# Kernel optimization log

Hardware: AMD Instinct MI355X
Metric: run time of the kernel (lower is better)

## Reference

```python
import jax, jax.numpy as jnp
import numpy as np

EPS = 1e-5
V, D, S, B, H, DH, FF, LE, LD = 32000, 512, 1024, 2, 8, 64, 2048, 2, 2


def _ln(x, g, b):
    m = x.mean(-1, keepdims=True)
    v = ((x - m) ** 2).mean(-1, keepdims=True)
    return (x - m) * jax.lax.rsqrt(v + EPS) * g + b


def _mha(qi, ki, vi, wq, wk, wv, uw, ub, mask):
    # wq/wk/wv: [H, D, DH] stacked per-head no-bias projections (concat order == head order)
    q = jnp.einsum('bsd,hde->bhse', qi, wq)
    k = jnp.einsum('btd,hde->bhte', ki, wk)
    v = jnp.einsum('btd,hde->bhte', vi, wv)
    scale = float(wq.shape[-1]) ** 0.5  # FAITHFUL to source: scores are MULTIPLIED by sqrt(d_head)
    s = jnp.einsum('bhse,bhte->bhst', q, k) * scale
    s = jnp.where(mask, s, -jnp.inf)  # causal tril mask applied in every attention (incl. cross)
    a = jax.nn.softmax(s, axis=-1)
    o = jnp.einsum('bhst,bhte->bhse', a, v)
    b_, h_, s_, e_ = o.shape
    o = o.transpose(0, 2, 1, 3).reshape(b_, s_, h_ * e_)
    return o @ uw + ub


def _posenc(seq, d):
    pos = jnp.arange(seq, dtype=jnp.float32)[:, None]
    den = jnp.exp(jnp.arange(0, d, 2, dtype=jnp.float32) * (-np.log(10000.0) / d))
    pe = jnp.zeros((seq, d), jnp.float32)
    pe = pe.at[:, 0::2].set(jnp.sin(pos * den))
    pe = pe.at[:, 1::2].set(jnp.cos(pos * den))
    return pe


def _forward(tokens, emb, enc_wq, enc_wk, enc_wv, enc_uo_w, enc_uo_b,
             enc_ln1_g, enc_ln1_b, enc_ln2_g, enc_ln2_b,
             enc_ff_w1, enc_ff_b1, enc_ff_w2, enc_ff_b2,
             dec_sa_wq, dec_sa_wk, dec_sa_wv, dec_sa_uo_w, dec_sa_uo_b,
             dec_ca_wq, dec_ca_wk, dec_ca_wv, dec_ca_uo_w, dec_ca_uo_b,
             dec_ln1_g, dec_ln1_b, dec_ln2_g, dec_ln2_b, dec_ln3_g, dec_ln3_b,
             dec_ff_w1, dec_ff_b1, dec_ff_w2, dec_ff_b2,
             ln_enc_g, ln_enc_b, ln_dec_g, ln_dec_b, head_w, head_b):
    b, s = tokens.shape
    d = emb.shape[1]
    x = emb[tokens] + _posenc(s, d)  # [B, S, D]
    mask = jnp.tril(jnp.ones((s, s), bool))
    enc = jax.lax.stop_gradient(x)  # source: x.detach().clone()
    for l in range(enc_wq.shape[0]):
        h = _ln(enc, enc_ln1_g[l], enc_ln1_b[l])
        enc = enc + _mha(h, h, h, enc_wq[l], enc_wk[l], enc_wv[l], enc_uo_w[l], enc_uo_b[l], mask)
        h = _ln(enc, enc_ln2_g[l], enc_ln2_b[l])
        enc = enc + (jnp.maximum(h @ enc_ff_w1[l] + enc_ff_b1[l], 0.0) @ enc_ff_w2[l] + enc_ff_b2[l])
    enc = _ln(enc, ln_enc_g, ln_enc_b)
    for l in range(dec_sa_wq.shape[0]):
        h = _ln(x, dec_ln1_g[l], dec_ln1_b[l])
        x = x + _mha(h, h, h, dec_sa_wq[l], dec_sa_wk[l], dec_sa_wv[l], dec_sa_uo_w[l], dec_sa_uo_b[l], mask)
        h = _ln(x, dec_ln2_g[l], dec_ln2_b[l])
        x = x + _mha(h, enc, enc, dec_ca_wq[l], dec_ca_wk[l], dec_ca_wv[l], dec_ca_uo_w[l], dec_ca_uo_b[l], mask)
        h = _ln(x, dec_ln3_g[l], dec_ln3_b[l])
        x = x + (jnp.maximum(h @ dec_ff_w1[l] + dec_ff_b1[l], 0.0) @ dec_ff_w2[l] + dec_ff_b2[l])
    x = _ln(x, ln_dec_g, ln_dec_b)
    return x @ head_w + head_b  # [B, S, V]


def setup_inputs():
    key = jax.random.key(0)
    ks = iter(jax.random.split(key, 64))
    def n(shape):
        return jax.random.normal(next(ks), shape, jnp.float32) * 0.02
    return {
        'tokens': jax.random.randint(next(ks), (B, S), 0, V, jnp.int32),
        'emb': n((V, D)),
        'enc_wq': n((LE, H, D, DH)), 'enc_wk': n((LE, H, D, DH)), 'enc_wv': n((LE, H, D, DH)),
        'enc_uo_w': n((LE, D, D)), 'enc_uo_b': jnp.zeros((LE, D), jnp.float32),
        'enc_ln1_g': jnp.ones((LE, D), jnp.float32), 'enc_ln1_b': jnp.zeros((LE, D), jnp.float32),
        'enc_ln2_g': jnp.ones((LE, D), jnp.float32), 'enc_ln2_b': jnp.zeros((LE, D), jnp.float32),
        'enc_ff_w1': n((LE, D, FF)), 'enc_ff_b1': jnp.zeros((LE, FF), jnp.float32),
        'enc_ff_w2': n((LE, FF, D)), 'enc_ff_b2': jnp.zeros((LE, D), jnp.float32),
        'dec_sa_wq': n((LD, H, D, DH)), 'dec_sa_wk': n((LD, H, D, DH)), 'dec_sa_wv': n((LD, H, D, DH)),
        'dec_sa_uo_w': n((LD, D, D)), 'dec_sa_uo_b': jnp.zeros((LD, D), jnp.float32),
        'dec_ca_wq': n((LD, H, D, DH)), 'dec_ca_wk': n((LD, H, D, DH)), 'dec_ca_wv': n((LD, H, D, DH)),
        'dec_ca_uo_w': n((LD, D, D)), 'dec_ca_uo_b': jnp.zeros((LD, D), jnp.float32),
        'dec_ln1_g': jnp.ones((LD, D), jnp.float32), 'dec_ln1_b': jnp.zeros((LD, D), jnp.float32),
        'dec_ln2_g': jnp.ones((LD, D), jnp.float32), 'dec_ln2_b': jnp.zeros((LD, D), jnp.float32),
        'dec_ln3_g': jnp.ones((LD, D), jnp.float32), 'dec_ln3_b': jnp.zeros((LD, D), jnp.float32),
        'dec_ff_w1': n((LD, D, FF)), 'dec_ff_b1': jnp.zeros((LD, FF), jnp.float32),
        'dec_ff_w2': n((LD, FF, D)), 'dec_ff_b2': jnp.zeros((LD, D), jnp.float32),
        'ln_enc_g': jnp.ones((D,), jnp.float32), 'ln_enc_b': jnp.zeros((D,), jnp.float32),
        'ln_dec_g': jnp.ones((D,), jnp.float32), 'ln_dec_b': jnp.zeros((D,), jnp.float32),
        'head_w': n((D, V)), 'head_b': jnp.zeros((V,), jnp.float32),
    }


def reference(tokens, emb, enc_wq, enc_wk, enc_wv, enc_uo_w, enc_uo_b,
              enc_ln1_g, enc_ln1_b, enc_ln2_g, enc_ln2_b,
              enc_ff_w1, enc_ff_b1, enc_ff_w2, enc_ff_b2,
              dec_sa_wq, dec_sa_wk, dec_sa_wv, dec_sa_uo_w, dec_sa_uo_b,
              dec_ca_wq, dec_ca_wk, dec_ca_wv, dec_ca_uo_w, dec_ca_uo_b,
              dec_ln1_g, dec_ln1_b, dec_ln2_g, dec_ln2_b, dec_ln3_g, dec_ln3_b,
              dec_ff_w1, dec_ff_b1, dec_ff_w2, dec_ff_b2,
              ln_enc_g, ln_enc_b, ln_dec_g, ln_dec_b, head_w, head_b):
    return _forward(tokens, emb, enc_wq, enc_wk, enc_wv, enc_uo_w, enc_uo_b,
                    enc_ln1_g, enc_ln1_b, enc_ln2_g, enc_ln2_b,
                    enc_ff_w1, enc_ff_b1, enc_ff_w2, enc_ff_b2,
                    dec_sa_wq, dec_sa_wk, dec_sa_wv, dec_sa_uo_w, dec_sa_uo_b,
                    dec_ca_wq, dec_ca_wk, dec_ca_wv, dec_ca_uo_w, dec_ca_uo_b,
                    dec_ln1_g, dec_ln1_b, dec_ln2_g, dec_ln2_b, dec_ln3_g, dec_ln3_b,
                    dec_ff_w1, dec_ff_b1, dec_ff_w2, dec_ff_b2,
                    ln_enc_g, ln_enc_b, ln_dec_g, ln_dec_b, head_w, head_b)
```

## Files before the change

kernel.cpp:

```cpp
#include <hip/hip_runtime.h>
#include <cstddef>
#include <cstdint>

constexpr int Vv = 32000, Dd = 512, Ss = 1024, Bb = 2, Hh = 8, DHd = 64, FFf = 2048;
constexpr int Tt = Bb * Ss;
constexpr int QKVW = 3 * Dd;
constexpr float EPSf = 1e-5f;

typedef unsigned short ushort_t;
typedef short bf16x8 __attribute__((ext_vector_type(8)));
typedef short short4v __attribute__((ext_vector_type(4)));
typedef float f32x4 __attribute__((ext_vector_type(4)));

constexpr size_t AQKV = 0;
constexpr size_t AUO  = 4718592;
constexpr size_t AFF1 = 6291456;
constexpr size_t AFF2 = 10485760;
constexpr size_t AEND = 14680064;

__device__ __forceinline__ ushort_t f2b(float f) {
  unsigned int u = __float_as_uint(f);
  unsigned int r = (u + 0x7FFFu + ((u >> 16) & 1u)) >> 16;
  return (ushort_t)r;
}
__device__ __forceinline__ float bits2f(ushort_t u) {
  return __uint_as_float((unsigned int)u << 16);
}

__device__ __forceinline__ void st_out(float* p, float v) { *p = v; }
__device__ __forceinline__ void st_out(ushort_t* p, float v) { *p = f2b(v); }

__device__ __forceinline__ void gload_lds16(const void* g, void* l) {
  __builtin_amdgcn_global_load_lds(
      (const __attribute__((address_space(1))) unsigned int*)g,
      (__attribute__((address_space(3))) unsigned int*)l, 16, 0, 0);
}

__global__ __launch_bounds__(256) void prep_all_k(
    const float* __restrict__ ewq, const float* __restrict__ ewk, const float* __restrict__ ewv,
    const float* __restrict__ swq, const float* __restrict__ swk, const float* __restrict__ swv,
    const float* __restrict__ cwq, const float* __restrict__ cwk, const float* __restrict__ cwv,
    const float* __restrict__ euo, const float* __restrict__ suo, const float* __restrict__ cuo,
    const float* __restrict__ eff1, const float* __restrict__ dff1,
    const float* __restrict__ eff2, const float* __restrict__ dff2,
    ushort_t* __restrict__ arena,
    const int* __restrict__ tok, const float* __restrict__ emb,
    float* __restrict__ X, float* __restrict__ ENC,
    const float* __restrict__ headw, ushort_t* __restrict__ headDst) {
  int idx = blockIdx.x;

  if (idx >= 14336 && idx < 16384) {
    int row = idx - 14336;
    int s = row & (Ss - 1);
    int t = tok[row];
    const float* e = emb + (size_t)t * Dd;
    for (int d = threadIdx.x; d < Dd; d += 256) {
      int i = d >> 1;
      float den = expf(-(float)(2 * i) * (9.210340371976184f / 512.0f));
      float ang = (float)s * den;
      float pe = (d & 1) ? cosf(ang) : sinf(ang);
      float v = e[d] + pe;
      X[(size_t)row * Dd + d] = v;
      ENC[(size_t)row * Dd + d] = v;
    }
    return;
  }

  const float* src;
  ushort_t* dst;
  int R, C, tile;
  if (idx < 4608) {
    tile = idx & 31;
    int rest = idx >> 5;
    int h = rest & 7; rest >>= 3;
    int t = rest % 3, gl = rest / 3;
    int g = gl >> 1, l = gl & 1;
    const float* bq = (g == 0) ? ewq : (g == 1) ? swq : cwq;
    const float* bk = (g == 0) ? ewk : (g == 1) ? swk : cwk;
    const float* bv = (g == 0) ? ewv : (g == 1) ? swv : cwv;
    const float* base = (t == 0) ? bq : (t == 1) ? bk : bv;
    src = base + (size_t)l * (Hh * Dd * DHd) + (size_t)h * (Dd * DHd);
    dst = arena + AQKV + (size_t)gl * (QKVW * Dd) + ((size_t)t * Dd + h * DHd) * Dd;
    R = 512; C = 64;
  } else if (idx < 6144) {
    int i2 = idx - 4608;
    tile = i2 & 255;
    int gl = i2 >> 8;
    int g = gl >> 1, l = gl & 1;
    const float* base = (g == 0) ? euo : (g == 1) ? suo : cuo;
    src = base + (size_t)l * (Dd * Dd);
    dst = arena + AUO + (size_t)gl * (Dd * Dd);
    R = 512; C = 512;
  } else if (idx < 10240) {
    int i3 = idx - 6144;
    tile = i3 & 1023;
    int dl = i3 >> 10;
    int d = dl >> 1, l = dl & 1;
    src = (d ? dff1 : eff1) + (size_t)l * (Dd * FFf);
    dst = arena + AFF1 + (size_t)dl * (Dd * FFf);
    R = 512; C = 2048;
  } else if (idx < 14336) {
    int i4 = idx - 10240;
    tile = i4 & 1023;
    int dl = i4 >> 10;
    int d = dl >> 1, l = dl & 1;
    src = (d ? dff2 : eff2) + (size_t)l * (FFf * Dd);
    dst = arena + AFF2 + (size_t)dl * (FFf * Dd);
    R = 2048; C = 512;
  } else {
    tile = idx - 16384;
    src = headw; dst = headDst;
    R = 512; C = 32000;
  }
  int nR = R >> 5;
  int r0 = (tile % nR) * 32, c0 = (tile / nR) * 32;
  __shared__ float tb[32][33];
  int tx = threadIdx.x & 31, ty = threadIdx.x >> 5;
#pragma unroll
  for (int i = 0; i < 4; i++)
    tb[ty + i * 8][tx] = src[(size_t)(r0 + ty + i * 8) * C + c0 + tx];
  __syncthreads();
#pragma unroll
  for (int i = 0; i < 4; i++)
    dst[(size_t)(c0 + ty + i * 8) * R + r0 + tx] = f2b(tb[tx][ty + i * 8]);
}

__global__ __launch_bounds__(256) void tcast_k(const float* __restrict__ in,
                                               ushort_t* __restrict__ out,
                                               int R, int C) {
  __shared__ float t[32][33];
  int c0 = blockIdx.x * 32, r0 = blockIdx.y * 32;
  int tx = threadIdx.x & 31, ty = threadIdx.x >> 5;
#pragma unroll
  for (int i = 0; i < 4; i++)
    t[ty + i * 8][tx] = in[(size_t)(r0 + ty + i * 8) * C + c0 + tx];
  __syncthreads();
#pragma unroll
  for (int i = 0; i < 4; i++)
    out[(size_t)(c0 + ty + i * 8) * R + r0 + tx] = f2b(t[tx][ty + i * 8]);
}

__global__ __launch_bounds__(256) void ln2_k(const float* __restrict__ in0,
                                             const float* __restrict__ g0,
                                             const float* __restrict__ b0,
                                             ushort_t* __restrict__ o0,
                                             const float* __restrict__ in1,
                                             const float* __restrict__ g1,
                                             const float* __restrict__ b1,
                                             ushort_t* __restrict__ o1,
                                             int nblk0) {
  int row = blockIdx.x;
  const float* in = in0; const float* g = g0; const float* b = b0; ushort_t* out = o0;
  if (row >= nblk0) { row -= nblk0; in = in1; g = g1; b = b1; out = o1; }
  const float* x = in + (size_t)row * Dd;
  int tid = threadIdx.x;
  float v0 = x[tid], v1 = x[tid + 256];
  float s = v0 + v1, ss = v0 * v0 + v1 * v1;
  for (int o = 32; o; o >>= 1) {
    s  += __shfl_down(s, o, 64);
    ss += __shfl_down(ss, o, 64);
  }
  __shared__ float rs[4], rss[4];
  int wid = tid >> 6, lane = tid & 63;
  if (lane == 0) { rs[wid] = s; rss[wid] = ss; }
  __syncthreads();
  __shared__ float mean_s, inv_s;
  if (tid == 0) {
    float a = rs[0] + rs[1] + rs[2] + rs[3];
    float c = rss[0] + rss[1] + rss[2] + rss[3];
    float m = a / Dd;
    float var = c / Dd - m * m;
    mean_s = m;
    inv_s = rsqrtf(var + EPSf);
  }
  __syncthreads();
  float m = mean_s, inv = inv_s;
  out[(size_t)row * Dd + tid]       = f2b((v0 - m) * inv * g[tid]       + b[tid]);
  out[(size_t)row * Dd + tid + 256] = f2b((v1 - m) * inv * g[tid + 256] + b[tid + 256]);
}

__device__ __forceinline__ void block_coords(int o, int nwg, bool nmajor,
                                             int nbM, int nbN, int& bmOut, int& bnOut) {
  int q = nwg >> 3, r = nwg & 7;
  int x = o & 7, i = o >> 3;
  int l = (x < r ? x * (q + 1) : r * (q + 1) + (x - r) * q) + i;
  int mb, nb;
  if (nmajor) { mb = l % nbM; nb = l / nbM; }
  else        { nb = l % nbN; mb = l / nbN; }
  bmOut = mb; bnOut = nb;
}

struct GD {
  const ushort_t* A; const ushort_t* BT; const float* bias; const float* resid;
  void* C; int N; int K; int ldc; int nbM; int nbN; int nwg;
};

template <int BM, int BN, bool NMAJOR, typename OutT, bool RELU>
__global__ __launch_bounds__(256) void gemm2_k(GD d0, GD d1, int nblk0) {
  constexpr int FM = BM / 32, FN = BN / 32;
  __shared__ __align__(16) ushort_t As[BM * 64];
  __shared__ __align__(16) ushort_t Bs[BN * 64];

  GD d = d0;
  int o = blockIdx.x;
  if (o >= nblk0) { d = d1; o -= nblk0; }
  int mb, nb;
  block_coords(o, d.nwg, NMAJOR, d.nbM, d.nbN, mb, nb);
  int bm = mb * BM, bn = nb * BN;
  int K = d.K, ldc = d.ldc;
  OutT* C = (OutT*)d.C;

  int tid = threadIdx.x;
  int lane = tid & 63, w = tid >> 6;
  int wr = w >> 1, wc = w & 1;
  f32x4 acc[FM][FN];
#pragma unroll
  for (int m = 0; m < FM; m++)
#pragma unroll
    for (int n = 0; n < FN; n++) acc[m][n] = (f32x4){0.f, 0.f, 0.f, 0.f};

  const ushort_t* aBase = d.A + (size_t)bm * K;
  const ushort_t* bBase = d.BT + (size_t)bn * K;
  int lr = lane & 15;
  int lk = (lane >> 4) * 8;

  for (int k0 = 0; k0 < K; k0 += 64) {
    __syncthreads();
#pragma unroll
    for (int it = 0; it < BM / 32; it++) {
      int cid = it * 256 + tid;
      int row = cid >> 3, c8 = cid & 7;
      int sc8 = c8 ^ (row & 7);
      gload_lds16(aBase + (size_t)row * K + k0 + sc8 * 8, &As[cid * 8]);
    }
#pragma unroll
    for (int it = 0; it < BN / 32; it++) {
      int cid = it * 256 + tid;
      int row = cid >> 3, c8 = cid & 7;
      int sc8 = c8 ^ (row & 7);
      gload_lds16(bBase + (size_t)row * K + k0 + sc8 * 8, &Bs[cid * 8]);
    }
    __syncthreads();
#pragma unroll
    for (int kk = 0; kk < 64; kk += 32) {
      bf16x8 af[FM], bfr[FN];
#pragma unroll
      for (int m = 0; m < FM; m++) {
        int row = wr * (BM / 2) + m * 16 + lr;
        af[m] = *(const bf16x8*)&As[row * 64 + ((kk + lk) ^ ((row & 7) << 3))];
      }
#pragma unroll
      for (int n = 0; n < FN; n++) {
        int row = wc * (BN / 2) + n * 16 + lr;
        bfr[n] = *(const bf16x8*)&Bs[row * 64 + ((kk + lk) ^ ((row & 7) << 3))];
      }
#pragma unroll
      for (int m = 0; m < FM; m++)
#pragma unroll
        for (int n = 0; n < FN; n++)
          acc[m][n] = __builtin_amdgcn_mfma_f32_16x16x32_bf16(af[m], bfr[n], acc[m][n], 0, 0, 0);
    }
  }

  int rowg = (lane >> 4) * 4;
#pragma unroll
  for (int m = 0; m < FM; m++) {
    int row0 = bm + wr * (BM / 2) + m * 16 + rowg;
#pragma unroll
    for (int n = 0; n < FN; n++) {
      int col = bn + wc * (BN / 2) + n * 16 + lr;
      float bv = d.bias ? d.bias[col] : 0.0f;
#pragma unroll
      for (int rr = 0; rr < 4; rr++) {
        int row = row0 + rr;
        float v = acc[m][n][rr] + bv;
        if (d.resid) v += d.resid[(size_t)row * ldc + col];
        if (RELU)  v = fmaxf(v, 0.0f);
        st_out(&C[(size_t)row * ldc + col], v);
      }
    }
  }
}

__global__ __launch_bounds__(128) void fattn_k(const float* __restrict__ QKV0,
                                               ushort_t* __restrict__ AO0,
                                               const float* __restrict__ QKV1,
                                               ushort_t* __restrict__ AO1,
                                               int nblk0) {
  int bid = blockIdx.x;
  const float* QKV = QKV0; ushort_t* AO = AO0;
  if (bid >= nblk0) { bid -= nblk0; QKV = QKV1; AO = AO1; }
  int i4 = bid >> 4;
  int qt = (i4 < 16) ? (31 - i4) : (i4 - 16);
  int h  = bid & 7;
  int b  = (bid >> 3) & 1;
  int q0 = qt * 32;
  int tid = threadIdx.x;
  int lane = tid & 63, w = tid >> 6;
  int g = lane >> 4, c = lane & 15;

  __shared__ __align__(16) ushort_t Qh[32 * 64], Ql[32 * 64];
  __shared__ __align__(16) ushort_t Kh[64 * 64], Kl[64 * 64];
  __shared__ __align__(16) ushort_t VT[64 * 64];
  __shared__ __align__(16) ushort_t Ps[2][16 * 64];

  {
    int row = tid >> 2, c0 = (tid & 3) * 16;
    const float* qb = QKV + ((size_t)(b * Ss + q0 + row) * QKVW + h * DHd + c0);
#pragma unroll
    for (int ii = 0; ii < 4; ii++) {
      float4 v = *(const float4*)(qb + ii * 4);
      int col = c0 + ii * 4;
      int sc = col ^ ((row & 7) << 3);
      ushort_t h0 = f2b(v.x), h1 = f2b(v.y), h2 = f2b(v.z), h3 = f2b(v.w);
      short4v hv = {(short)h0, (short)h1, (short)h2, (short)h3};
      short4v lv = {(short)f2b(v.x - bits2f(h0)), (short)f2b(v.y - bits2f(h1)),
                    (short)f2b(v.z - bits2f(h2)), (short)f2b(v.w - bits2f(h3))};
      *(short4v*)&Qh[row * 64 + sc] = hv;
      *(short4v*)&Ql[row * 64 + sc] = lv;
    }
  }

  f32x4 Oa[4];
#pragma unroll
  for (int n = 0; n < 4; n++) Oa[n] = (f32x4){0.f, 0.f, 0.f, 0.f};
  float mrow[4] = {-INFINITY, -INFINITY, -INFINITY, -INFINITY};
  float lrow[4] = {0.f, 0.f, 0.f, 0.f};

  int nkv = (qt >> 1) + 1;
  for (int it = 0; it < nkv; it++) {
    int t0 = it * 64;
    __syncthreads();
    {
      int row = tid >> 1, c0 = (tid & 1) * 32;
      const float* kb = QKV + ((size_t)(b * Ss + t0 + row) * QKVW + Dd + h * DHd + c0);
      const float* vb = kb + Dd;
#pragma unroll
      for (int ii = 0; ii < 8; ii++) {
        float4 v = *(const float4*)(kb + ii * 4);
        int col = c0 + ii * 4;
        int sc = col ^ ((row & 7) << 3);
        ushort_t h0 = f2b(v.x), h1 = f2b(v.y), h2 = f2b(v.z), h3 = f2b(v.w);
        short4v hv = {(short)h0, (short)h1, (short)h2, (short)h3};
        short4v lv = {(short)f2b(v.x - bits2f(h0)), (short)f2b(v.y - bits2f(h1)),
                      (short)f2b(v.z - bits2f(h2)), (short)f2b(v.w - bits2f(h3))};
        *(short4v*)&Kh[row * 64 + sc] = hv;
        *(short4v*)&Kl[row * 64 + sc] = lv;
      }
#pragma unroll
      for (int ii = 0; ii < 8; ii++) {
        float4 v = *(const float4*)(vb + ii * 4);
        int e0 = c0 + ii * 4;
        VT[(e0 + 0) * 64 + (row ^ (((e0 + 0) & 7) << 3))] = f2b(v.x);
        VT[(e0 + 1) * 64 + (row ^ (((e0 + 1) & 7) << 3))] = f2b(v.y);
        VT[(e0 + 2) * 64 + (row ^ (((e0 + 2) & 7) << 3))] = f2b(v.z);
        VT[(e0 + 3) * 64 + (row ^ (((e0 + 3) & 7) << 3))] = f2b(v.w);
      }
    }
    __syncthreads();

    int arow = w * 16 + c;
    int ksw0 = (0 + g * 8) ^ ((c & 7) << 3);
    int ksw1 = (32 + g * 8) ^ ((c & 7) << 3);
    bf16x8 qh0 = *(const bf16x8*)&Qh[arow * 64 + ksw0];
    bf16x8 qh1 = *(const bf16x8*)&Qh[arow * 64 + ksw1];
    bf16x8 ql0 = *(const bf16x8*)&Ql[arow * 64 + ksw0];
    bf16x8 ql1 = *(const bf16x8*)&Ql[arow * 64 + ksw1];

    f32x4 sfr[4];
#pragma unroll
    for (int n = 0; n < 4; n++) {
      int brow = n * 16 + c;
      bf16x8 kh0 = *(const bf16x8*)&Kh[brow * 64 + ksw0];
      bf16x8 kh1 = *(const bf16x8*)&Kh[brow * 64 + ksw1];
      bf16x8 kl0 = *(const bf16x8*)&Kl[brow * 64 + ksw0];
      bf16x8 kl1 = *(const bf16x8*)&Kl[brow * 64 + ksw1];
      f32x4 a = (f32x4){0.f, 0.f, 0.f, 0.f};
      a = __builtin_amdgcn_mfma_f32_16x16x32_bf16(qh0, kl0, a, 0, 0, 0);
      a = __builtin_amdgcn_mfma_f32_16x16x32_bf16(qh1, kl1, a, 0, 0, 0);
      a = __builtin_amdgcn_mfma_f32_16x16x32_bf16(ql0, kh0, a, 0, 0, 0);
      a = __builtin_amdgcn_mfma_f32_16x16x32_bf16(ql1, kh1, a, 0, 0, 0);
      a = __builtin_amdgcn_mfma_f32_16x16x32_bf16(qh0, kh0, a, 0, 0, 0);
      a = __builtin_amdgcn_mfma_f32_16x16x32_bf16(qh1, kh1, a, 0, 0, 0);
      sfr[n] = a;
    }

#pragma unroll
    for (int n = 0; n < 4; n++) {
#pragma unroll
      for (int rr = 0; rr < 4; rr++) sfr[n][rr] *= 8.0f;
    }
    if (it == nkv - 1) {
#pragma unroll
      for (int n = 0; n < 4; n++) {
        int t = t0 + n * 16 + c;
#pragma unroll
        for (int rr = 0; rr < 4; rr++) {
          int s = q0 + w * 16 + g * 4 + rr;
          if (t > s) sfr[n][rr] = -INFINITY;
        }
      }
    }

    float pnew[4], scold[4];
#pragma unroll
    for (int rr = 0; rr < 4; rr++) {
      float tm = fmaxf(fmaxf(sfr[0][rr], sfr[1][rr]), fmaxf(sfr[2][rr], sfr[3][rr]));
      tm = fmaxf(tm, __shfl_xor(tm, 1));
      tm = fmaxf(tm, __shfl_xor(tm, 2));
      tm = fmaxf(tm, __shfl_xor(tm, 4));
      tm = fmaxf(tm, __shfl_xor(tm, 8));
      float mn = fmaxf(mrow[rr], tm);
      scold[rr] = __expf(mrow[rr] - mn);
      mrow[rr] = mn;
      pnew[rr] = mn;
    }
#pragma unroll
    for (int n = 0; n < 4; n++) {
#pragma unroll
      for (int rr = 0; rr < 4; rr++) sfr[n][rr] = __expf(sfr[n][rr] - pnew[rr]);
    }
#pragma unroll
    for (int rr = 0; rr < 4; rr++) {
      float s = sfr[0][rr] + sfr[1][rr] + sfr[2][rr] + sfr[3][rr];
      s += __shfl_xor(s, 1);
      s += __shfl_xor(s, 2);
      s += __shfl_xor(s, 4);
      s += __shfl_xor(s, 8);
      lrow[rr] = lrow[rr] * scold[rr] + s;
    }

#pragma unroll
    for (int n = 0; n < 4; n++) {
#pragma unroll
      for (int rr = 0; rr < 4; rr++) {
        int prow = g * 4 + rr;
        Ps[w][prow * 64 + ((n * 16 + c) ^ ((prow & 7) << 3))] = f2b(sfr[n][rr]);
      }
    }

#pragma unroll
    for (int n = 0; n < 4; n++) {
#pragma unroll
      for (int rr = 0; rr < 4; rr++) Oa[n][rr] *= scold[rr];
    }

    bf16x8 pa0 = *(const bf16x8*)&Ps[w][c * 64 + ksw0];
    bf16x8 pa1 = *(const bf16x8*)&Ps[w][c * 64 + ksw1];
#pragma unroll
    for (int n = 0; n < 4; n++) {
      int vrow = n * 16 + c;
      bf16x8 v0 = *(const bf16x8*)&VT[vrow * 64 + ksw0];
      bf16x8 v1 = *(const bf16x8*)&VT[vrow * 64 + ksw1];
      Oa[n] = __builtin_amdgcn_mfma_f32_16x16x32_bf16(pa0, v0, Oa[n], 0, 0, 0);
      Oa[n] = __builtin_amdgcn_mfma_f32_16x16x32_bf16(pa1, v1, Oa[n], 0, 0, 0);
    }
  }

#pragma unroll
  for (int rr = 0; rr < 4; rr++) {
    float inv = 1.0f / lrow[rr];
    int row = b * Ss + q0 + w * 16 + g * 4 + rr;
#pragma unroll
    for (int n = 0; n < 4; n++) {
      AO[(size_t)row * Dd + h * DHd + n * 16 + c] = f2b(Oa[n][rr] * inv);
    }
  }
}

static GD mkGD(const ushort_t* A, const ushort_t* BT, const float* bias,
               const float* resid, void* C, int M, int N, int K, int ldc,
               int BM, int BN) {
  GD d;
  d.A = A; d.BT = BT; d.bias = bias; d.resid = resid; d.C = C;
  d.N = N; d.K = K; d.ldc = ldc;
  d.nbM = M / BM; d.nbN = N / BN; d.nwg = d.nbM * d.nbN;
  return d;
}

template <int BM, int BN, bool NMAJOR, typename OutT, bool RELU>
static void gemm1(hipStream_t st, GD d) {
  gemm2_k<BM, BN, NMAJOR, OutT, RELU><<<dim3(d.nwg), dim3(256), 0, st>>>(d, d, d.nwg);
}
template <int BM, int BN, bool NMAJOR, typename OutT, bool RELU>
static void gemm2(hipStream_t st, GD d0, GD d1) {
  gemm2_k<BM, BN, NMAJOR, OutT, RELU><<<dim3(d0.nwg + d1.nwg), dim3(256), 0, st>>>(d0, d1, d0.nwg);
}

extern "C" void kernel_launch(void* const* d_in, const int* in_sizes, int n_in,
                              void* d_out, int out_size, void* d_ws, size_t ws_size,
                              hipStream_t stream) {
  const int*   tokens    = (const int*)d_in[0];
  const float* emb       = (const float*)d_in[1];
  const float* enc_wq    = (const float*)d_in[2];
  const float* enc_wk    = (const float*)d_in[3];
  const float* enc_wv    = (const float*)d_in[4];
  const float* enc_uo_w  = (const float*)d_in[5];
  const float* enc_uo_b  = (const float*)d_in[6];
  const float* enc_ln1_g = (const float*)d_in[7];
  const float* enc_ln1_b = (const float*)d_in[8];
  const float* enc_ln2_g = (const float*)d_in[9];
  const float* enc_ln2_b = (const float*)d_in[10];
  const float* enc_ff_w1 = (const float*)d_in[11];
  const float* enc_ff_b1 = (const float*)d_in[12];
  const float* enc_ff_w2 = (const float*)d_in[13];
  const float* enc_ff_b2 = (const float*)d_in[14];
  const float* dec_sa_wq = (const float*)d_in[15];
  const float* dec_sa_wk = (const float*)d_in[16];
  const float* dec_sa_wv = (const float*)d_in[17];
  const float* dec_sa_uo_w = (const float*)d_in[18];
  const float* dec_sa_uo_b = (const float*)d_in[19];
  const float* dec_ca_wq = (const float*)d_in[20];
  const float* dec_ca_wk = (const float*)d_in[21];
  const float* dec_ca_wv = (const float*)d_in[22];
  const float* dec_ca_uo_w = (const float*)d_in[23];
  const float* dec_ca_uo_b = (const float*)d_in[24];
  const float* dec_ln1_g = (const float*)d_in[25];
  const float* dec_ln1_b = (const float*)d_in[26];
  const float* dec_ln2_g = (const float*)d_in[27];
  const float* dec_ln2_b = (const float*)d_in[28];
  const float* dec_ln3_g = (const float*)d_in[29];
  const float* dec_ln3_b = (const float*)d_in[30];
  const float* dec_ff_w1 = (const float*)d_in[31];
  const float* dec_ff_b1 = (const float*)d_in[32];
  const float* dec_ff_w2 = (const float*)d_in[33];
  const float* dec_ff_b2 = (const float*)d_in[34];
  const float* ln_enc_g  = (const float*)d_in[35];
  const float* ln_enc_b  = (const float*)d_in[36];
  const float* ln_dec_g  = (const float*)d_in[37];
  const float* ln_dec_b  = (const float*)d_in[38];
  const float* head_w    = (const float*)d_in[39];
  const float* head_b    = (const float*)d_in[40];
  float* out = (float*)d_out;

  char* ws = (char*)d_ws;
  size_t off = 0;
  auto alloc = [&](size_t bytes) {
    void* p = ws + off;
    off += (bytes + 255) & ~(size_t)255;
    return p;
  };
  ushort_t* Hb    = (ushort_t*)alloc((size_t)Tt * Dd * 2);
  ushort_t* Hb2   = (ushort_t*)alloc((size_t)Tt * Dd * 2);
  ushort_t* ENCFb = (ushort_t*)alloc((size_t)Tt * Dd * 2);
  float*    X     = (float*)alloc((size_t)Tt * Dd * 4);
  float*    ENC   = (float*)alloc((size_t)Tt * Dd * 4);
  float*    QKV   = (float*)alloc((size_t)Tt * QKVW * 4);
  float*    QKV2  = (float*)alloc((size_t)Tt * QKVW * 4);
  ushort_t* AO    = (ushort_t*)alloc((size_t)Tt * Dd * 2);
  ushort_t* AO2   = (ushort_t*)alloc((size_t)Tt * Dd * 2);
  ushort_t* Fb    = (ushort_t*)alloc((size_t)Tt * FFf * 2);
  ushort_t* ARENA = (ushort_t*)alloc(AEND * 2);

  size_t headBytes = (size_t)Vv * Dd * 2;
  bool headInPrep = (off + headBytes) <= ws_size;
  ushort_t* BThead = headInPrep ? (ushort_t*)alloc(headBytes) : (ushort_t*)X;

  dim3 blk(256), fblk(128);
  int attnB = Bb * Hh * (Ss / 32);

  {
    int nprep = 14336 + 2048 + (headInPrep ? 16000 : 0);
    prep_all_k<<<nprep, blk, 0, stream>>>(
        enc_wq, enc_wk, enc_wv, dec_sa_wq, dec_sa_wk, dec_sa_wv,
        dec_ca_wq, dec_ca_wk, dec_ca_wv,
        enc_uo_w, dec_sa_uo_w, dec_ca_uo_w,
        enc_ff_w1, dec_ff_w1, enc_ff_w2, dec_ff_w2, ARENA,
        tokens, emb, X, ENC, head_w, headInPrep ? BThead : nullptr);
  }

  auto BTq  = [&](int gl) { return ARENA + AQKV + (size_t)gl * (QKVW * Dd); };
  auto BTu  = [&](int gl) { return ARENA + AUO  + (size_t)gl * (Dd * Dd); };
  auto BT1  = [&](int dl) { return ARENA + AFF1 + (size_t)dl * (Dd * FFf); };
  auto BT2  = [&](int dl) { return ARENA + AFF2 + (size_t)dl * (FFf * Dd); };

  ln2_k<<<2 * Tt, blk, 0, stream>>>(ENC, enc_ln1_g, enc_ln1_b, Hb,
                                    X, dec_ln1_g, dec_ln1_b, Hb2, Tt);
  gemm2<64, 128, true, float, false>(stream,
      mkGD(Hb,  BTq(0), nullptr, nullptr, QKV,  Tt, QKVW, Dd, QKVW, 64, 128),
      mkGD(Hb2, BTq(2), nullptr, nullptr, QKV2, Tt, QKVW, Dd, QKVW, 64, 128));
  fattn_k<<<2 * attnB, fblk, 0, stream>>>(QKV, AO, QKV2, AO2, attnB);
  gemm2<64, 64, true, float, false>(stream,
      mkGD(AO,  BTu(0), enc_uo_b,    ENC, ENC, Tt, Dd, Dd, Dd, 64, 64),
      mkGD(AO2, BTu(2), dec_sa_uo_b, X,   X,   Tt, Dd, Dd, Dd, 64, 64));
  ln2_k<<<Tt, blk, 0, stream>>>(ENC, enc_ln2_g, enc_ln2_b, Hb, ENC, enc_ln2_g, enc_ln2_b, Hb, Tt);
  gemm1<64, 128, true, ushort_t, true>(stream,
      mkGD(Hb, BT1(0), enc_ff_b1, nullptr, Fb, Tt, FFf, Dd, FFf, 64, 128));
  gemm1<64, 64, false, float, false>(stream,
      mkGD(Fb, BT2(0), enc_ff_b2, ENC, ENC, Tt, Dd, FFf, Dd, 64, 64));

  ln2_k<<<Tt, blk, 0, stream>>>(ENC, enc_ln1_g + Dd, enc_ln1_b + Dd, Hb,
                                ENC, enc_ln1_g + Dd, enc_ln1_b + Dd, Hb, Tt);
  gemm1<64, 128, true, float, false>(stream,
      mkGD(Hb, BTq(1), nullptr, nullptr, QKV, Tt, QKVW, Dd, QKVW, 64, 128));
  fattn_k<<<attnB, fblk, 0, stream>>>(QKV, AO, QKV, AO, attnB);
  gemm1<64, 64, true, float, false>(stream,
      mkGD(AO, BTu(1), enc_uo_b + Dd, ENC, ENC, Tt, Dd, Dd, Dd, 64, 64));
  ln2_k<<<Tt, blk, 0, stream>>>(ENC, enc_ln2_g + Dd, enc_ln2_b + Dd, Hb,
                                ENC, enc_ln2_g + Dd, enc_ln2_b + Dd, Hb, Tt);
  gemm1<64, 128, true, ushort_t, true>(stream,
      mkGD(Hb, BT1(1), enc_ff_b1 + FFf, nullptr, Fb, Tt, FFf, Dd, FFf, 64, 128));
  gemm1<64, 64, false, float, false>(stream,
      mkGD(Fb, BT2(1), enc_ff_b2 + Dd, ENC, ENC, Tt, Dd, FFf, Dd, 64, 64));

  for (int l = 0; l < 2; l++) {
    if (l == 0) {
      ln2_k<<<2 * Tt, blk, 0, stream>>>(ENC, ln_enc_g, ln_enc_b, ENCFb,
                                        X, dec_ln2_g, dec_ln2_b, Hb, Tt);
    } else {
      ln2_k<<<Tt, blk, 0, stream>>>(X, dec_ln1_g + Dd, dec_ln1_b + Dd, Hb,
                                    X, dec_ln1_g + Dd, dec_ln1_b + Dd, Hb, Tt);
      gemm1<64, 128, true, float, false>(stream,
          mkGD(Hb, BTq(3), nullptr, nullptr, QKV, Tt, QKVW, Dd, QKVW, 64, 128));
      fattn_k<<<attnB, fblk, 0, stream>>>(QKV, AO, QKV, AO, attnB);
      gemm1<64, 64, true, float, false>(stream,
          mkGD(AO, BTu(3), dec_sa_uo_b + Dd, X, X, Tt, Dd, Dd, Dd, 64, 64));
      ln2_k<<<Tt, blk, 0, stream>>>(X, dec_ln2_g + Dd, dec_ln2_b + Dd, Hb,
                                    X, dec_ln2_g + Dd, dec_ln2_b + Dd, Hb, Tt);
    }
    const ushort_t* BTca = BTq(4 + l);
    gemm2<64, 128, true, float, false>(stream,
        mkGD(Hb,    BTca,                    nullptr, nullptr, QKV,      Tt, Dd,     Dd, QKVW, 64, 128),
        mkGD(ENCFb, BTca + (size_t)Dd * Dd,  nullptr, nullptr, QKV + Dd, Tt, 2 * Dd, Dd, QKVW, 64, 128));
    fattn_k<<<attnB, fblk, 0, stream>>>(QKV, AO, QKV, AO, attnB);
    gemm1<64, 64, true, float, false>(stream,
        mkGD(AO, BTu(4 + l), dec_ca_uo_b + l * Dd, X, X, Tt, Dd, Dd, Dd, 64, 64));
    ln2_k<<<Tt, blk, 0, stream>>>(X, dec_ln3_g + l * Dd, dec_ln3_b + l * Dd, Hb,
                                  X, dec_ln3_g + l * Dd, dec_ln3_b + l * Dd, Hb, Tt);
    gemm1<64, 128, true, ushort_t, true>(stream,
        mkGD(Hb, BT1(2 + l), dec_ff_b1 + l * FFf, nullptr, Fb, Tt, FFf, Dd, FFf, 64, 128));
    gemm1<64, 64, false, float, false>(stream,
        mkGD(Fb, BT2(2 + l), dec_ff_b2 + l * Dd, X, X, Tt, Dd, FFf, Dd, 64, 64));
  }
  ln2_k<<<Tt, blk, 0, stream>>>(X, ln_dec_g, ln_dec_b, Hb, X, ln_dec_g, ln_dec_b, Hb, Tt);

  if (!headInPrep)
    tcast_k<<<dim3(Vv / 32, Dd / 32), blk, 0, stream>>>(head_w, BThead, Dd, Vv);
  gemm1<128, 128, true, float, false>(stream,
      mkGD(Hb, BThead, head_b, nullptr, out, Tt, Vv, Dd, Vv, 128, 128));
}
```

Measured before the change: 741.3 us.

## Widen GEMM K-tile and co-schedule encoder FFN with decoder cross-attn Q

The GEMM kernel gains a BK template parameter, and most projection and FFN GEMMs now use a 128-wide K tile, which halves the number of K-loop iterations and barriers. ReLU and bf16 output become runtime flags instead of template parameters, so different epilogues can share one launch. The decoder's first-layer cross-attention Q projection is now batched with the encoder's first FFN1 GEMM, and its LayerNorm is batched with the encoder ln2, which cuts launches and fills the GPU better. In exchange, shared memory per block doubles, which may lower occupancy, and the epilogue gains runtime branches.

Result: no change. 741.3 us (median of 2 runs) (-0.0%).

```diff
diff --git a/kernel.cpp b/kernel.cpp
--- a/kernel.cpp
+++ b/kernel.cpp
@@ -26,9 +26,6 @@
 __device__ __forceinline__ float bits2f(ushort_t u) {
   return __uint_as_float((unsigned int)u << 16);
 }
-
-__device__ __forceinline__ void st_out(float* p, float v) { *p = v; }
-__device__ __forceinline__ void st_out(ushort_t* p, float v) { *p = f2b(v); }
 
 __device__ __forceinline__ void gload_lds16(const void* g, void* l) {
   __builtin_amdgcn_global_load_lds(
@@ -192,14 +189,15 @@
 
 struct GD {
   const ushort_t* A; const ushort_t* BT; const float* bias; const float* resid;
-  void* C; int N; int K; int ldc; int nbM; int nbN; int nwg;
+  void* C; int N; int K; int ldc; int nbM; int nbN; int nwg; int relu; int obf16;
 };
 
-template <int BM, int BN, bool NMAJOR, typename OutT, bool RELU>
+template <int BM, int BN, int BK, bool NMAJOR>
 __global__ __launch_bounds__(256) void gemm2_k(GD d0, GD d1, int nblk0) {
   constexpr int FM = BM / 32, FN = BN / 32;
-  __shared__ __align__(16) ushort_t As[BM * 64];
-  __shared__ __align__(16) ushort_t Bs[BN * 64];
+  constexpr int KG = BK / 8;
+  __shared__ __align__(16) ushort_t As[BM * BK];
+  __shared__ __align__(16) ushort_t Bs[BN * BK];
 
   GD d = d0;
   int o = blockIdx.x;
@@ -208,7 +206,6 @@
   block_coords(o, d.nwg, NMAJOR, d.nbM, d.nbN, mb, nb);
   int bm = mb * BM, bn = nb * BN;
   int K = d.K, ldc = d.ldc;
-  OutT* C = (OutT*)d.C;
 
   int tid = threadIdx.x;
   int lane = tid & 63, w = tid >> 6;
@@ -224,35 +221,35 @@
   int lr = lane & 15;
   int lk = (lane >> 4) * 8;
 
-  for (int k0 = 0; k0 < K; k0 += 64) {
+  for (int k0 = 0; k0 < K; k0 += BK) {
     __syncthreads();
 #pragma unroll
-    for (int it = 0; it < BM / 32; it++) {
+    for (int it = 0; it < (BM * BK) / 2048; it++) {
       int cid = it * 256 + tid;
-      int row = cid >> 3, c8 = cid & 7;
+      int row = cid / KG, c8 = cid % KG;
       int sc8 = c8 ^ (row & 7);
       gload_lds16(aBase + (size_t)row * K + k0 + sc8 * 8, &As[cid * 8]);
     }
 #pragma unroll
-    for (int it = 0; it < BN / 32; it++) {
+    for (int it = 0; it < (BN * BK) / 2048; it++) {
       int cid = it * 256 + tid;
-      int row = cid >> 3, c8 = cid & 7;
+      int row = cid / KG, c8 = cid % KG;
       int sc8 = c8 ^ (row & 7);
       gload_lds16(bBase + (size_t)row * K + k0 + sc8 * 8, &Bs[cid * 8]);
     }
     __syncthreads();
 #pragma unroll
-    for (int kk = 0; kk < 64; kk += 32) {
+    for (int kk = 0; kk < BK; kk += 32) {
       bf16x8 af[FM], bfr[FN];
 #pragma unroll
       for (int m = 0; m < FM; m++) {
         int row = wr * (BM / 2) + m * 16 + lr;
-        af[m] = *(const bf16x8*)&As[row * 64 + ((kk + lk) ^ ((row & 7) << 3))];
+        af[m] = *(const bf16x8*)&As[row * BK + ((kk + lk) ^ ((row & 7) << 3))];
       }
 #pragma unroll
       for (int n = 0; n < FN; n++) {
         int row = wc * (BN / 2) + n * 16 + lr;
-        bfr[n] = *(const bf16x8*)&Bs[row * 64 + ((kk + lk) ^ ((row & 7) << 3))];
+        bfr[n] = *(const bf16x8*)&Bs[row * BK + ((kk + lk) ^ ((row & 7) << 3))];
       }
 #pragma unroll
       for (int m = 0; m < FM; m++)
@@ -275,8 +272,9 @@
         int row = row0 + rr;
         float v = acc[m][n][rr] + bv;
         if (d.resid) v += d.resid[(size_t)row * ldc + col];
-        if (RELU)  v = fmaxf(v, 0.0f);
-        st_out(&C[(size_t)row * ldc + col], v);
+        if (d.relu)  v = fmaxf(v, 0.0f);
+        if (d.obf16) ((ushort_t*)d.C)[(size_t)row * ldc + col] = f2b(v);
+        else         ((float*)d.C)[(size_t)row * ldc + col] = v;
       }
     }
   }
@@ -470,21 +468,22 @@
 
 static GD mkGD(const ushort_t* A, const ushort_t* BT, const float* bias,
                const float* resid, void* C, int M, int N, int K, int ldc,
-               int BM, int BN) {
+               int BM, int BN, int relu, int obf16) {
   GD d;
   d.A = A; d.BT = BT; d.bias = bias; d.resid = resid; d.C = C;
   d.N = N; d.K = K; d.ldc = ldc;
   d.nbM = M / BM; d.nbN = N / BN; d.nwg = d.nbM * d.nbN;
+  d.relu = relu; d.obf16 = obf16;
   return d;
 }
 
-template <int BM, int BN, bool NMAJOR, typename OutT, bool RELU>
+template <int BM, int BN, int BK, bool NMAJOR>
 static void gemm1(hipStream_t st, GD d) {
-  gemm2_k<BM, BN, NMAJOR, OutT, RELU><<<dim3(d.nwg), dim3(256), 0, st>>>(d, d, d.nwg);
-}
-template <int BM, int BN, bool NMAJOR, typename OutT, bool RELU>
+  gemm2_k<BM, BN, BK, NMAJOR><<<dim3(d.nwg), dim3(256), 0, st>>>(d, d, d.nwg);
+}
+template <int BM, int BN, int BK, bool NMAJOR>
 static void gemm2(hipStream_t st, GD d0, GD d1) {
-  gemm2_k<BM, BN, NMAJOR, OutT, RELU><<<dim3(d0.nwg + d1.nwg), dim3(256), 0, st>>>(d0, d1, d0.nwg);
+  gemm2_k<BM, BN, BK, NMAJOR><<<dim3(d0.nwg + d1.nwg), dim3(256), 0, st>>>(d0, d1, d0.nwg);
 }
 
 extern "C" void kernel_launch(void* const* d_in, const int* in_sizes, int n_in,
@@ -576,66 +575,76 @@
 
   ln2_k<<<2 * Tt, blk, 0, stream>>>(ENC, enc_ln1_g, enc_ln1_b, Hb,
                                     X, dec_ln1_g, dec_ln1_b, Hb2, Tt);
-  gemm2<64, 128, true, float, false>(stream,
-      mkGD(Hb,  BTq(0), nullptr, nullptr, QKV,  Tt, QKVW, Dd, QKVW, 64, 128),
-      mkGD(Hb2, BTq(2), nullptr, nullptr, QKV2, Tt, QKVW, Dd, QKVW, 64, 128));
+  gemm2<64, 128, 128, true>(stream,
+      mkGD(Hb,  BTq(0), nullptr, nullptr, QKV,  Tt, QKVW, Dd, QKVW, 64, 128, 0, 0),
+      mkGD(Hb2, BTq(2), nullptr, nullptr, QKV2, Tt, QKVW, Dd, QKVW, 64, 128, 0, 0));
   fattn_k<<<2 * attnB, fblk, 0, stream>>>(QKV, AO, QKV2, AO2, attnB);
-  gemm2<64, 64, true, float, false>(stream,
-      mkGD(AO,  BTu(0), enc_uo_b,    ENC, ENC, Tt, Dd, Dd, Dd, 64, 64),
-      mkGD(AO2, BTu(2), dec_sa_uo_b, X,   X,   Tt, Dd, Dd, Dd, 64, 64));
-  ln2_k<<<Tt, blk, 0, stream>>>(ENC, enc_ln2_g, enc_ln2_b, Hb, ENC, enc_ln2_g, enc_ln2_b, Hb, Tt);
-  gemm1<64, 128, true, ushort_t, true>(stream,
-      mkGD(Hb, BT1(0), enc_ff_b1, nullptr, Fb, Tt, FFf, Dd, FFf, 64, 128));
-  gemm1<64, 64, false, float, false>(stream,
-      mkGD(Fb, BT2(0), enc_ff_b2, ENC, ENC, Tt, Dd, FFf, Dd, 64, 64));
+  gemm2<64, 64, 128, true>(stream,
+      mkGD(AO,  BTu(0), enc_uo_b,    ENC, ENC, Tt, Dd, Dd, Dd, 64, 64, 0, 0),
+      mkGD(AO2, BTu(2), dec_sa_uo_b, X,   X,   Tt, Dd, Dd, Dd, 64, 64, 0, 0));
+  ln2_k<<<2 * Tt, blk, 0, stream>>>(ENC, enc_ln2_g, enc_ln2_b, Hb,
+                                    X, dec_ln2_g, dec_ln2_b, Hb2, Tt);
+  gemm2<64, 128, 128, true>(stream,
+      mkGD(Hb,  BT1(0), enc_ff_b1, nullptr, Fb,   Tt, FFf, Dd, FFf,  64, 128, 1, 1),
+      mkGD(Hb2, BTq(4), nullptr,   nullptr, QKV2, Tt, Dd,  Dd, QKVW, 64, 128, 0, 0));
+  gemm1<64, 64, 128, false>(stream,
+      mkGD(Fb, BT2(0), enc_ff_b2, ENC, ENC, Tt, Dd, FFf, Dd, 64, 64, 0, 0));
 
   ln2_k<<<Tt, blk, 0, stream>>>(ENC, enc_ln1_g + Dd, enc_ln1_b + Dd, Hb,
                                 ENC, enc_ln1_g + Dd, enc_ln1_b + Dd, Hb, Tt);
-  gemm1<64, 128, true, float, false>(stream,
-      mkGD(Hb, BTq(1), nullptr, nullptr, QKV, Tt, QKVW, Dd, QKVW, 64, 128));
+  gemm1<64, 128, 128, true>(stream,
+      mkGD(Hb, BTq(1), nullptr, nullptr, QKV, Tt, QKVW, Dd, QKVW, 64, 128, 0, 0));
   fattn_k<<<attnB, fblk, 0, stream>>>(QKV, AO, QKV, AO, attnB);
-  gemm1<64, 64, true, float, false>(stream,
-      mkGD(AO, BTu(1), enc_uo_b + Dd, ENC, ENC, Tt, Dd, Dd, Dd, 64, 64));
+  gemm1<64, 64, 128, true>(stream,
+      mkGD(AO, BTu(1), enc_uo_b + Dd, ENC, ENC, Tt, Dd, Dd, Dd, 64, 64, 0, 0));
   ln2_k<<<Tt, blk, 0, stream>>>(ENC, enc_ln2_g + Dd, enc_ln2_b + Dd, Hb,
                                 ENC, enc_ln2_g + Dd, enc_ln2_b + Dd, Hb, Tt);
-  gemm1<64, 128, true, ushort_t, true>(stream,
-      mkGD(Hb, BT1(1), enc_ff_b1 + FFf, nullptr, Fb, Tt, FFf, Dd, FFf, 64, 128));
-  gemm1<64, 64, false, float, false>(stream,
-      mkGD(Fb, BT2(1), enc_ff_b2 + Dd, ENC, ENC, Tt, Dd, FFf, Dd, 64, 64));
-
-  for (int l = 0; l < 2; l++) {
-    if (l == 0) {
-      ln2_k<<<2 * Tt, blk, 0, stream>>>(ENC, ln_enc_g, ln_enc_b, ENCFb,
-                                        X, dec_ln2_g, dec_ln2_b, Hb, Tt);
-    } else {
-      ln2_k<<<Tt, blk, 0, stream>>>(X, dec_ln1_g + Dd, dec_ln1_b + Dd, Hb,
-                                    X, dec_ln1_g + Dd, dec_ln1_b + Dd, Hb, Tt);
-      gemm1<64, 128, true, float, false>(stream,
-          mkGD(Hb, BTq(3), nullptr, nullptr, QKV, Tt, QKVW, Dd, QKVW, 64, 128));
-      fattn_k<<<attnB, fblk, 0, stream>>>(QKV, AO, QKV, AO, attnB);
-      gemm1<64, 64, true, float, false>(stream,
-          mkGD(AO, BTu(3), dec_sa_uo_b + Dd, X, X, Tt, Dd, Dd, Dd, 64, 64));
-      ln2_k<<<Tt, blk, 0, stream>>>(X, dec_ln2_g + Dd, dec_ln2_b + Dd, Hb,
-                                    X, dec_ln2_g + Dd, dec_ln2_b + Dd, Hb, Tt);
-    }
-    const ushort_t* BTca = BTq(4 + l);
-    gemm2<64, 128, true, float, false>(stream,
-        mkGD(Hb,    BTca,                    nullptr, nullptr, QKV,      Tt, Dd,     Dd, QKVW, 64, 128),
-        mkGD(ENCFb, BTca + (size_t)Dd * Dd,  nullptr, nullptr, QKV + Dd, Tt, 2 * Dd, Dd, QKVW, 64, 128));
-    fattn_k<<<attnB, fblk, 0, stream>>>(QKV, AO, QKV, AO, attnB);
-    gemm1<64, 64, true, float, false>(stream,
-        mkGD(AO, BTu(4 + l), dec_ca_uo_b + l * Dd, X, X, Tt, Dd, Dd, Dd, 64, 64));
-    ln2_k<<<Tt, blk, 0, stream>>>(X, dec_ln3_g + l * Dd, dec_ln3_b + l * Dd, Hb,
-                                  X, dec_ln3_g + l * Dd, dec_ln3_b + l * Dd, Hb, Tt);
-    gemm1<64, 128, true, ushort_t, true>(stream,
-        mkGD(Hb, BT1(2 + l), dec_ff_b1 + l * FFf, nullptr, Fb, Tt, FFf, Dd, FFf, 64, 128));
-    gemm1<64, 64, false, float, false>(stream,
-        mkGD(Fb, BT2(2 + l), dec_ff_b2 + l * Dd, X, X, Tt, Dd, FFf, Dd, 64, 64));
-  }
+  gemm1<64, 128, 128, true>(stream,
+      mkGD(Hb, BT1(1), enc_ff_b1 + FFf, nullptr, Fb, Tt, FFf, Dd, FFf, 64, 128, 1, 1));
+  gemm1<64, 64, 128, false>(stream,
+      mkGD(Fb, BT2(1), enc_ff_b2 + Dd, ENC, ENC, Tt, Dd, FFf, Dd, 64, 64, 0, 0));
+
+  ln2_k<<<Tt, blk, 0, stream>>>(ENC, ln_enc_g, ln_enc_b, ENCFb,
+                                ENC, ln_enc_g, ln_enc_b, ENCFb, Tt);
+  gemm1<64, 128, 128, true>(stream,
+      mkGD(ENCFb, BTq(4) + (size_t)Dd * Dd, nullptr, nullptr, QKV2 + Dd,
+           Tt, 2 * Dd, Dd, QKVW, 64, 128, 0, 0));
+  fattn_k<<<attnB, fblk, 0, stream>>>(QKV2, AO2, QKV2, AO2, attnB);
+  gemm1<64, 64, 128, true>(stream,
+      mkGD(AO2, BTu(4), dec_ca_uo_b, X, X, Tt, Dd, Dd, Dd, 64, 64, 0, 0));
+  ln2_k<<<Tt, blk, 0, stream>>>(X, dec_ln3_g, dec_ln3_b, Hb,
+                                X, dec_ln3_g, dec_ln3_b, Hb, Tt);
+  gemm1<64, 128, 128, true>(stream,
+      mkGD(Hb, BT1(2), dec_ff_b1, nullptr, Fb, Tt, FFf, Dd, FFf, 64, 128, 1, 1));
+  gemm1<64, 64, 128, false>(stream,
+      mkGD(Fb, BT2(2), dec_ff_b2, X, X, Tt, Dd, FFf, Dd, 64, 64, 0, 0));
+
+  ln2_k<<<Tt, blk, 0, stream>>>(X, dec_ln1_g + Dd, dec_ln1_b + Dd, Hb,
+                                X, dec_ln1_g + Dd, dec_ln1_b + Dd, Hb, Tt);
+  gemm1<64, 128, 128, true>(stream,
+      mkGD(Hb, BTq(3), nullptr, nullptr, QKV, Tt, QKVW, Dd, QKVW, 64, 128, 0, 0));
+  fattn_k<<<attnB, fblk, 0, stream>>>(QKV, AO, QKV, AO, attnB);
+  gemm1<64, 64, 128, true>(stream,
+      mkGD(AO, BTu(3), dec_sa_uo_b + Dd, X, X, Tt, Dd, Dd, Dd, 64, 64, 0, 0));
+  ln2_k<<<Tt, blk, 0, stream>>>(X, dec_ln2_g + Dd, dec_ln2_b + Dd, Hb,
+                                X, dec_ln2_g + Dd, dec_ln2_b + Dd, Hb, Tt);
+  gemm2<64, 128, 128, true>(stream,
+      mkGD(Hb,    BTq(5),                    nullptr, nullptr, QKV,      Tt, Dd,     Dd, QKVW, 64, 128, 0, 0),
+      mkGD(ENCFb, BTq(5) + (size_t)Dd * Dd,  nullptr, nullptr, QKV + Dd, Tt, 2 * Dd, Dd, QKVW, 64, 128, 0, 0));
+  fattn_k<<<attnB, fblk, 0, stream>>>(QKV, AO, QKV, AO, attnB);
+  gemm1<64, 64, 128, true>(stream,
+      mkGD(AO, BTu(5), dec_ca_uo_b + Dd, X, X, Tt, Dd, Dd, Dd, 64, 64, 0, 0));
+  ln2_k<<<Tt, blk, 0, stream>>>(X, dec_ln3_g + Dd, dec_ln3_b + Dd, Hb,
+                                X, dec_ln3_g + Dd, dec_ln3_b + Dd, Hb, Tt);
+  gemm1<64, 128, 128, true>(stream,
+      mkGD(Hb, BT1(3), dec_ff_b1 + FFf, nullptr, Fb, Tt, FFf, Dd, FFf, 64, 128, 1, 1));
+  gemm1<64, 64, 128, false>(stream,
+      mkGD(Fb, BT2(3), dec_ff_b2 + Dd, X, X, Tt, Dd, FFf, Dd, 64, 64, 0, 0));
+
   ln2_k<<<Tt, blk, 0, stream>>>(X, ln_dec_g, ln_dec_b, Hb, X, ln_dec_g, ln_dec_b, Hb, Tt);
 
   if (!headInPrep)
     tcast_k<<<dim3(Vv / 32, Dd / 32), blk, 0, stream>>>(head_w, BThead, Dd, Vv);
-  gemm1<128, 128, true, float, false>(stream,
-      mkGD(Hb, BThead, head_b, nullptr, out, Tt, Vv, Dd, Vv, 128, 128));
-}
+  gemm1<128, 128, 64, true>(stream,
+      mkGD(Hb, BThead, head_b, nullptr, out, Tt, Vv, Dd, Vv, 128, 128, 0, 0));
+}
```
